# Performance work log

Hardware: AMD Instinct MI355X
Metric: run time of the kernel (lower is better)

Reference implementation:

```python
import jax, jax.numpy as jnp
import numpy as np

B, T, D = 8, 1024, 512
H = 8
F_OUT = D // H          # 64 per head
ALPHA = 0.2             # LeakyReLU slope in GAT
MASK_RATE = 0.3
GAMMA = 0.0625          # DistanceAdj gamma
BIAS = 0.2              # DistanceAdj bias
LN_EPS = 1e-5
NEG_INF = -9e15
L2_EPS = 1e-12          # F.normalize eps


def setup_inputs() -> dict:
    key = jax.random.key(0)
    ks = jax.random.split(key, 8)
    return {
        "x": jax.random.normal(ks[0], (B, T, D), jnp.float32),
        "W": jax.random.normal(ks[1], (H, D, F_OUT), jnp.float32) * 0.05,
        "a_src": jax.random.normal(ks[2], (H, F_OUT), jnp.float32) * 0.05,
        "a_dst": jax.random.normal(ks[3], (H, F_OUT), jnp.float32) * 0.05,
        "W2": jax.random.normal(ks[4], (D, D), jnp.float32) * 0.02,
        "b2": jnp.zeros((D,), jnp.float32),
        "ln_g": jnp.ones((D,), jnp.float32),
        "ln_b": jnp.zeros((D,), jnp.float32),
    }


def _distance_adj(batch, t):
    # DistanceAdj: Gaussian kernel over temporal index distance, shared across batch
    idx = jnp.arange(t, dtype=jnp.float32)
    d2 = (idx[:, None] - idx[None, :]) ** 2
    adj = jnp.exp(-GAMMA * d2 - BIAS)                      # [T, T]
    return jnp.broadcast_to(adj[None], (batch, t, t))      # [B, T, T]


def reference(x, W, a_src, a_dst, W2, b2, ln_g, ln_b):
    b, t, d = x.shape
    adj = _distance_adj(b, t)

    # top-k magnitude node selection -> row/col union mask (index_fill loop)
    k = int(MASK_RATE * t)
    mags = jnp.linalg.norm(x, axis=2)                      # [B, T]
    _, topk = jax.lax.top_k(mags, k)                       # [B, k]
    sel = jnp.zeros((b, t), bool).at[jnp.arange(b)[:, None], topk].set(True)
    mask = sel[:, :, None] | sel[:, None, :]               # rows OR cols filled
    adj = jnp.where(mask, adj, 0.0)

    # GAT multi-head attention (dense masked form, dropout=0 at eval)
    Wh = jnp.einsum("btd,hdf->bhtf", x, W)                 # [B,H,T,F']
    e_src = jnp.einsum("bhtf,hf->bht", Wh, a_src)
    e_dst = jnp.einsum("bhtf,hf->bht", Wh, a_dst)
    e = jax.nn.leaky_relu(e_src[..., :, None] + e_dst[..., None, :], ALPHA)
    e = jnp.where(adj[:, None] > 0, e, NEG_INF)            # masked logits
    attn = jax.nn.softmax(e, axis=-1)                      # [B,H,T,T]
    hp = jnp.einsum("bhts,bhsf->bhtf", attn, Wh)
    hp = jax.nn.elu(hp)                                    # concat=True -> elu per head
    tmp = hp.transpose(0, 2, 1, 3).reshape(b, t, d)        # concat heads -> [B,T,512]

    # signed-sqrt + F.normalize (default dim=1 -> over T axis)
    tmp = jnp.sqrt(jax.nn.relu(tmp)) - jnp.sqrt(jax.nn.relu(-tmp))
    nrm = jnp.linalg.norm(tmp, axis=1, keepdims=True)      # [B,1,D]
    tmp = tmp / jnp.maximum(nrm, L2_EPS)

    # residual linear + LayerNorm + permute
    y = x + tmp @ W2 + b2
    mu = jnp.mean(y, axis=-1, keepdims=True)
    var = jnp.mean((y - mu) ** 2, axis=-1, keepdims=True)
    y = (y - mu) / jnp.sqrt(var + LN_EPS) * ln_g + ln_b
    return y.transpose(0, 2, 1)                            # [B, D, T]
```

## Files before the change

### kernel.cpp

```cpp
#include <hip/hip_runtime.h>
#include <hip/hip_bf16.h>

typedef unsigned short u16;
typedef short bf16x8 __attribute__((ext_vector_type(8)));
typedef float f32x4 __attribute__((ext_vector_type(4)));
typedef int   i32x4 __attribute__((ext_vector_type(4)));

#define NB 8
#define NT 1024
#define ND 512
#define KSEL 307
#define PSTR 152
#define TSTR 136

__device__ __forceinline__ float bf2f(u16 u){
  union { unsigned int i; float f; } c; c.i = ((unsigned int)u) << 16; return c.f;
}
__device__ __forceinline__ u16 f2bf(float f){
  __hip_bfloat16 h = __float2bfloat16(f);
  u16 u; __builtin_memcpy(&u, &h, 2); return u;
}

__global__ void k_select(const float* __restrict__ mags, int* __restrict__ sel){
  __shared__ float sm[NT];
  int b = blockIdx.x;
  int tid = threadIdx.x;
  for (int i = tid; i < NT; i += 256) sm[i] = mags[b * NT + i];
  __syncthreads();
  int tl = tid >> 2, tq = tid & 3;
  int t = blockIdx.y * 64 + tl;
  float m = sm[t];
  int cnt = 0;
  int s0 = tq * 256;
  for (int s = s0; s < s0 + 256; s++){
    float v = sm[s];
    cnt += (v > m) || (v == m && s < t);
  }
  cnt += __shfl_xor(cnt, 1, 64);
  cnt += __shfl_xor(cnt, 2, 64);
  if (tq == 0) sel[b * NT + t] = (cnt < KSEL) ? 1 : 0;
}

__launch_bounds__(256, 3)
__global__ void k_gemm_wh(const float* __restrict__ x, const float* __restrict__ Wf,
                          const float* __restrict__ W2f,
                          const float* __restrict__ a_src, const float* __restrict__ a_dst,
                          u16* __restrict__ WhT, float* __restrict__ es, float* __restrict__ ed,
                          float* __restrict__ mags, float* __restrict__ cn,
                          u16* __restrict__ W2T){
  __shared__ u16 smem[8704];
  u16* As = smem;
  u16* Bs = smem + 5120;
  int m0 = blockIdx.x * 128;
  int h  = blockIdx.y;
  int tid = threadIdx.x;
  if (h == 0 && tid < 64) cn[blockIdx.x * 64 + tid] = 0.f;
  if (h == 2){
    float* tile = (float*)smem;
    int kt0 = (blockIdx.x >> 3) * 64, n00 = (blockIdx.x & 7) * 64;
    int r = tid >> 6, cl = tid & 63;
#pragma unroll
    for (int p = 0; p < 16; p++)
      tile[(r + p*4)*65 + cl] = W2f[(size_t)(kt0 + r + p*4) * 512 + n00 + cl];
    __syncthreads();
#pragma unroll
    for (int p = 0; p < 16; p++){
      int orow = r + p*4;
      W2T[(size_t)(n00 + orow) * 512 + kt0 + cl] = f2bf(tile[cl*65 + orow]);
    }
    __syncthreads();
  }
  int wv = tid >> 6, lane = tid & 63;
  int quad = lane >> 4, lr = lane & 15;
  f32x4 acc[2][4] = {};
  float sq[2] = {0.f, 0.f};
  int ar = (tid * 8) >> 5, ac = (tid * 8) & 31;
  const float* xa0 = &x[(size_t)(m0 + ar) * 512 + ac];
  const float* xa1 = xa0 + (size_t)64 * 512;
  int kk = (tid * 8) >> 6, f0 = (tid * 8) & 63;
  const float* wb = &Wf[((size_t)h << 15) + (size_t)kk * 64 + f0];
  int bbase = f0 * 40 + (((kk >> 3) ^ ((f0 >> 3) & 3)) * 8) + (kk & 7);
  f32x4 pa0 = *(const f32x4*)xa0, pa1 = *(const f32x4*)(xa0 + 4);
  f32x4 pa2 = *(const f32x4*)xa1, pa3 = *(const f32x4*)(xa1 + 4);
  f32x4 pb0 = *(const f32x4*)wb,  pb1 = *(const f32x4*)(wb + 4);
  for (int kt = 0; kt < 512; kt += 32){
    __syncthreads();
    {
      u16 pk[8];
      if (h == 0){
#pragma unroll
        for (int q = 0; q < 4; q++) sq[0] += pa0[q]*pa0[q] + pa1[q]*pa1[q];
#pragma unroll
        for (int q = 0; q < 4; q++) sq[1] += pa2[q]*pa2[q] + pa3[q]*pa3[q];
      }
#pragma unroll
      for (int q = 0; q < 4; q++){ pk[q] = f2bf(pa0[q]); pk[4+q] = f2bf(pa1[q]); }
      *(bf16x8*)&As[ar*40 + ac] = *(const bf16x8*)pk;
#pragma unroll
      for (int q = 0; q < 4; q++){ pk[q] = f2bf(pa2[q]); pk[4+q] = f2bf(pa3[q]); }
      *(bf16x8*)&As[(ar + 64)*40 + ac] = *(const bf16x8*)pk;
#pragma unroll
      for (int q = 0; q < 4; q++) Bs[bbase + q*40]       = f2bf(pb0[q]);
#pragma unroll
      for (int q = 0; q < 4; q++) Bs[bbase + (q+4)*40]   = f2bf(pb1[q]);
    }
    __syncthreads();
    if (kt < 480){
      pa0 = *(const f32x4*)(xa0 + kt + 32); pa1 = *(const f32x4*)(xa0 + kt + 36);
      pa2 = *(const f32x4*)(xa1 + kt + 32); pa3 = *(const f32x4*)(xa1 + kt + 36);
      pb0 = *(const f32x4*)(wb + (size_t)(kt + 32) * 64);
      pb1 = *(const f32x4*)(wb + (size_t)(kt + 32) * 64 + 4);
    }
    bf16x8 af[2], bfr[4];
#pragma unroll
    for (int i = 0; i < 2; i++) af[i] = *(const bf16x8*)&As[(wv*32 + i*16 + lr)*40 + quad*8];
#pragma unroll
    for (int i = 0; i < 4; i++){
      int f = i*16 + lr;
      bfr[i] = *(const bf16x8*)&Bs[f*40 + ((quad ^ ((f >> 3) & 3)) * 8)];
    }
#pragma unroll
    for (int mi = 0; mi < 2; mi++)
#pragma unroll
      for (int ni = 0; ni < 4; ni++)
        acc[mi][ni] = __builtin_amdgcn_mfma_f32_16x16x32_bf16(af[mi], bfr[ni], acc[mi][ni], 0, 0, 0);
  }
  if (h == 0){
#pragma unroll
    for (int i = 0; i < 2; i++){
      float s = sq[i];
      s += __shfl_xor(s, 1, 64);
      s += __shfl_xor(s, 2, 64);
      if ((tid & 3) == 0) mags[m0 + i*64 + (tid >> 2)] = sqrtf(s);
    }
  }
  float asv[4], adv[4];
#pragma unroll
  for (int ni = 0; ni < 4; ni++){
    asv[ni] = a_src[h*64 + ni*16 + lr];
    adv[ni] = a_dst[h*64 + ni*16 + lr];
  }
#pragma unroll
  for (int mi = 0; mi < 2; mi++)
#pragma unroll
    for (int r = 0; r < 4; r++){
      float pes = 0.f, ped = 0.f;
#pragma unroll
      for (int ni = 0; ni < 4; ni++){
        pes += acc[mi][ni][r] * asv[ni];
        ped += acc[mi][ni][r] * adv[ni];
      }
#pragma unroll
      for (int mofs = 1; mofs < 16; mofs <<= 1){
        pes += __shfl_xor(pes, mofs, 64);
        ped += __shfl_xor(ped, mofs, 64);
      }
      if (lr == 0){
        int rowg = m0 + wv*32 + mi*16 + quad*4 + r;
        int bb_ = rowg >> 10, tt = rowg & 1023;
        es[(bb_ * 8 + h) * NT + tt] = pes;
        ed[(bb_ * 8 + h) * NT + tt] = ped;
      }
    }
  __syncthreads();
  u16* Tr = smem;
#pragma unroll
  for (int mi = 0; mi < 2; mi++)
#pragma unroll
    for (int ni = 0; ni < 4; ni++){
      int fl = ni*16 + lr;
      int tl = wv*32 + mi*16 + quad*4;
#pragma unroll
      for (int r = 0; r < 4; r++) Tr[fl*TSTR + tl + r] = f2bf(acc[mi][ni][r]);
    }
  __syncthreads();
  int f = tid >> 2, seg = tid & 3;
  int b_ = m0 >> 10;
  u16* dst = &WhT[(b_ * 512 + h * 64 + f) * NT + (m0 & 1023) + seg*32];
  const u16* srcp = &Tr[f*TSTR + seg*32];
#pragma unroll
  for (int k8 = 0; k8 < 4; k8++)
    *(bf16x8*)(dst + k8*8) = *(const bf16x8*)(srcp + k8*8);
}

__launch_bounds__(256)
__global__ void k_attn(const u16* __restrict__ WhT, const float* __restrict__ es,
                       const float* __restrict__ ed, const int* __restrict__ sel,
                       u16* __restrict__ t2b, float* __restrict__ cn){
  __shared__ u16 P[64 * PSTR];
  __shared__ float edw[144];
  __shared__ int   selw[144];
  __shared__ float esw[64];
  __shared__ float swv[64];
  int bh = blockIdx.x;
  int b = bh >> 3;
  int t0 = blockIdx.y * 64;
  int tid = threadIdx.x;
  int wv = tid >> 6, lane = tid & 63;
  int quad = lane >> 4, lr = lane & 15;
  int s_base = t0 - 40;
  for (int i = tid; i < 144; i += 256){
    int s = s_base + i;
    bool ok = (s >= 0 && s < NT);
    edw[i]  = ok ? ed[bh * NT + s] : 0.f;
    selw[i] = ok ? sel[b * NT + s] : 0;
  }
  if (tid < 64) esw[tid] = es[bh * NT + t0 + tid];
  {
    i32x4 z = {};
    for (int i = lane; i < 304; i += 64){
      int r16 = i / 19, c16 = i - r16 * 19;
      *(i32x4*)&P[(16*wv + r16) * PSTR + c16 * 8] = z;
    }
  }
  __syncthreads();
  {
    int tl = 16*wv + (lane >> 2);
    int q = lane & 3;
    float e_t = esw[tl];
    int sel_t = selw[tl + 40];
    float part = 0.f;
    for (int j = q; j <= 80; j += 4){
      int sw = tl + j;
      int s = s_base + sw;
      float w = 0.f;
      if (s >= 0 && s < NT && (sel_t | selw[sw])){
        float v = e_t + edw[sw];
        v = v > 0.f ? v : 0.2f * v;
        v = fminf(v, 60.f);
        w = bf2f(f2bf(__expf(v)));
      }
      part += w;
      if (w != 0.f) P[tl * PSTR + sw] = f2bf(w);
    }
    part += __shfl_xor(part, 1, 64);
    part += __shfl_xor(part, 2, 64);
    if (q == 0) swv[tl] = part;
  }
  __syncthreads();
  f32x4 acc[4] = {};
  const u16* vbase = WhT + (bh * 64) * NT;
#pragma unroll
  for (int ks = 0; ks < 96; ks += 32){
    bf16x8 afr = *(const bf16x8*)&P[(16*wv + lr) * PSTR + 16*wv + ks + quad*8];
    int tb = s_base + 16*wv + ks + quad*8;
    bool ok = (tb >= 0) && (tb < NT);
    bf16x8 zf = {};
#pragma unroll
    for (int jn = 0; jn < 4; jn++){
      bf16x8 bfr = ok ? *(const bf16x8*)&vbase[(16*jn + lr) * NT + tb] : zf;
      acc[jn] = __builtin_amdgcn_mfma_f32_16x16x32_bf16(afr, bfr, acc[jn], 0, 0, 0);
    }
  }
#pragma unroll
  for (int jn = 0; jn < 4; jn++){
    float ssum = 0.f;
#pragma unroll
    for (int r = 0; r < 4; r++){
      int t_loc = 16*wv + quad*4 + r;
      float sw_ = swv[t_loc];
      float hp = acc[jn][r] / (sw_ > 0.f ? sw_ : 1.f);
      hp = hp > 0.f ? hp : (__expf(hp) - 1.f);
      float o = hp >= 0.f ? sqrtf(hp) : -sqrtf(-hp);
      ssum += o * o;
      t2b[(b * NT + t0 + t_loc) * ND + (bh & 7) * 64 + 16*jn + lr] = f2bf(o);
    }
    ssum += __shfl_xor(ssum, 16, 64);
    ssum += __shfl_xor(ssum, 32, 64);
    if (quad == 0) atomicAdd(&cn[b * ND + (bh & 7) * 64 + 16*jn + lr], ssum);
  }
}

__launch_bounds__(512)
__global__ void k_gemm2ln(const u16* __restrict__ A, const u16* __restrict__ W2T,
                          const float* __restrict__ xres, const float* __restrict__ b2,
                          const float* __restrict__ cn, const float* __restrict__ g,
                          const float* __restrict__ bb, float* __restrict__ out){
  __shared__ __align__(16) char smraw[69888];
  u16*   As  = (u16*)smraw;
  u16*   Bs  = (u16*)(smraw + 2560);
  float* scl = (float*)(smraw + 43520);
  float* T     = (float*)smraw;
  float* wpart = (float*)(smraw + 67584);
  float* mus   = (float*)(smraw + 69632);
  float* rss   = (float*)(smraw + 69760);
  int tid = threadIdx.x;
  int m0 = blockIdx.x * 32;
  int b  = m0 >> 10, t0 = m0 & 1023;
  int w = tid >> 6, lane = tid & 63;
  int quad = lane >> 4, lr = lane & 15;
  {
    float nv = sqrtf(cn[(b << 9) + tid]);
    scl[tid] = 1.f / fmaxf(nv, 1e-12f);
  }
  int ar = tid >> 2, ac = (tid & 3) * 8;
  const u16* ap = &A[(size_t)(m0 + ar) * 512 + ac];
  int nb_ = tid >> 2, c = (tid & 3) * 8;
  bf16x8 ra = {}, rb[4];
  if (tid < 128) ra = *(const bf16x8*)ap;
#pragma unroll
  for (int rep = 0; rep < 4; rep++)
    rb[rep] = *(const bf16x8*)&W2T[(size_t)(nb_ + rep*128) * 512 + c];
  f32x4 acc[2][4] = {};
  for (int kt = 0; kt < 512; kt += 32){
    __syncthreads();
    if (tid < 128){
      u16 pk[8];
#pragma unroll
      for (int q = 0; q < 8; q++)
        pk[q] = f2bf(bf2f((u16)ra[q]) * scl[kt + ac + q]);
      *(bf16x8*)&As[ar*40 + ac] = *(const bf16x8*)pk;
    }
#pragma unroll
    for (int rep = 0; rep < 4; rep++)
      *(bf16x8*)&Bs[(nb_ + rep*128)*40 + c] = rb[rep];
    __syncthreads();
    if (kt < 480){
      if (tid < 128) ra = *(const bf16x8*)(ap + kt + 32);
#pragma unroll
      for (int rep = 0; rep < 4; rep++)
        rb[rep] = *(const bf16x8*)&W2T[(size_t)(nb_ + rep*128) * 512 + kt + 32 + c];
    }
    bf16x8 af[2], bfr[4];
#pragma unroll
    for (int mi = 0; mi < 2; mi++) af[mi] = *(const bf16x8*)&As[(mi*16 + lr)*40 + quad*8];
#pragma unroll
    for (int i = 0; i < 4; i++)
      bfr[i] = *(const bf16x8*)&Bs[(w*64 + i*16 + lr)*40 + quad*8];
#pragma unroll
    for (int mi = 0; mi < 2; mi++)
#pragma unroll
      for (int ni = 0; ni < 4; ni++)
        acc[mi][ni] = __builtin_amdgcn_mfma_f32_16x16x32_bf16(af[mi], bfr[ni], acc[mi][ni], 0, 0, 0);
  }
  float b2v[4];
#pragma unroll
  for (int ni = 0; ni < 4; ni++) b2v[ni] = b2[w*64 + ni*16 + lr];
  float yv[2][4][4];
#pragma unroll
  for (int mi = 0; mi < 2; mi++)
#pragma unroll
    for (int r = 0; r < 4; r++){
      int rl = mi*16 + quad*4 + r;
      float rs = 0.f, rq = 0.f;
#pragma unroll
      for (int ni = 0; ni < 4; ni++){
        int col = w*64 + ni*16 + lr;
        float v = acc[mi][ni][r] + xres[(size_t)(m0 + rl) * 512 + col] + b2v[ni];
        yv[mi][ni][r] = v;
        rs += v; rq += v * v;
      }
#pragma unroll
      for (int m2 = 1; m2 < 16; m2 <<= 1){
        rs += __shfl_xor(rs, m2, 64);
        rq += __shfl_xor(rq, m2, 64);
      }
      if (lr == 0){
        wpart[w*32 + rl]       = rs;
        wpart[256 + w*32 + rl] = rq;
      }
    }
  __syncthreads();
  if (tid < 32){
    float s = 0.f, q = 0.f;
#pragma unroll
    for (int wv2 = 0; wv2 < 8; wv2++){
      s += wpart[wv2*32 + tid];
      q += wpart[256 + wv2*32 + tid];
    }
    float mu = s * (1.f/512.f);
    float var = q * (1.f/512.f) - mu * mu;
    mus[tid] = mu;
    rss[tid] = 1.f / sqrtf(var + 1e-5f);
  }
  __syncthreads();
  float gv[4], bv[4];
#pragma unroll
  for (int ni = 0; ni < 4; ni++){
    gv[ni] = g[w*64 + ni*16 + lr];
    bv[ni] = bb[w*64 + ni*16 + lr];
  }
#pragma unroll
  for (int mi = 0; mi < 2; mi++)
#pragma unroll
    for (int r = 0; r < 4; r++){
      int rl = mi*16 + quad*4 + r;
      float mu = mus[rl], rstd = rss[rl];
#pragma unroll
      for (int ni = 0; ni < 4; ni++){
        int col = w*64 + ni*16 + lr;
        T[col*33 + rl] = (yv[mi][ni][r] - mu) * rstd * gv[ni] + bv[ni];
      }
    }
  __syncthreads();
  int j = tid & 31, dq = tid >> 5;
#pragma unroll
  for (int kk2 = 0; kk2 < 32; kk2++){
    int d = dq + kk2 * 16;
    out[((size_t)(b * 512 + d)) * 1024 + t0 + j] = T[d*33 + j];
  }
}

extern "C" void kernel_launch(void* const* d_in, const int* in_sizes, int n_in,
                              void* d_out, int out_size, void* d_ws, size_t ws_size,
                              hipStream_t stream) {
  (void)in_sizes; (void)n_in; (void)out_size; (void)ws_size;
  const float* x     = (const float*)d_in[0];
  const float* W     = (const float*)d_in[1];
  const float* a_src = (const float*)d_in[2];
  const float* a_dst = (const float*)d_in[3];
  const float* W2    = (const float*)d_in[4];
  const float* b2    = (const float*)d_in[5];
  const float* ln_g  = (const float*)d_in[6];
  const float* ln_b  = (const float*)d_in[7];
  char* ws = (char*)d_ws;
  int*   sel   = (int*)  (ws + 256);
  float* mags  = (float*)(ws + 33024);
  float* es    = (float*)(ws + 1124608);
  float* ed    = (float*)(ws + 1386752);
  float* cn    = (float*)(ws + 1648896);
  u16*   WhT   = (u16*)  (ws + 2097152);
  u16*   t2b   = (u16*)  (ws + 18874368);
  u16*   W2T   = (u16*)  (ws + 36175872);
  float* out   = (float*)d_out;

  k_gemm_wh  <<<dim3(64, 8), 256, 0, stream>>>(x, W, W2, a_src, a_dst, WhT, es, ed, mags, cn, W2T);
  k_select   <<<dim3(NB, 16), 256, 0, stream>>>(mags, sel);
  k_attn     <<<dim3(64, 16), 256, 0, stream>>>(WhT, es, ed, sel, t2b, cn);
  k_gemm2ln  <<<dim3(256), 512, 0, stream>>>(t2b, W2T, x, b2, cn, ln_g, ln_b, out);
}
```

Measured before the change: 143.7 us.

## Add bf16 prep kernel and load MFMA fragments directly from global memory

A new prep kernel converts x to bf16, computes row magnitudes, zeroes the column-norm buffer, and transposes W and W2 into bf16 K-major layouts. The Wh GEMM and the W2 GEMM then drop their LDS staging and barriers, loading MFMA operand fragments straight from global memory with register double-buffering. The column scaling in the second GEMM is applied per fragment in registers. This removes per-iteration LDS writes and syncs and the fp32-to-bf16 conversion inside the GEMM loops. In exchange it adds an extra kernel launch and a pass over x in HBM, and operands are re-read from global or L2 with no LDS reuse across waves.

```diff
diff --git a/kernel.cpp b/kernel.cpp
--- a/kernel.cpp
+++ b/kernel.cpp
@@ -19,6 +19,60 @@
 __device__ __forceinline__ u16 f2bf(float f){
   __hip_bfloat16 h = __float2bfloat16(f);
   u16 u; __builtin_memcpy(&u, &h, 2); return u;
+}
+
+__global__ void k_prep(const float* __restrict__ x, const float* __restrict__ Wf,
+                       const float* __restrict__ W2f, u16* __restrict__ xbf,
+                       u16* __restrict__ WbT, u16* __restrict__ W2T,
+                       float* __restrict__ mags, float* __restrict__ cn){
+  __shared__ float tile[64][65];
+  int bx = blockIdx.x;
+  int tid = threadIdx.x;
+  if (bx < 512){
+    int wv = tid >> 6, lane = tid & 63;
+#pragma unroll
+    for (int rr = 0; rr < 4; rr++){
+      int row = bx * 16 + wv * 4 + rr;
+      const float* xp = &x[(size_t)row * 512 + lane * 8];
+      f32x4 u0 = *(const f32x4*)xp;
+      f32x4 u1 = *(const f32x4*)(xp + 4);
+      u16 pk[8];
+      float s = 0.f;
+#pragma unroll
+      for (int q = 0; q < 4; q++){
+        s += u0[q]*u0[q] + u1[q]*u1[q];
+        pk[q] = f2bf(u0[q]); pk[4+q] = f2bf(u1[q]);
+      }
+      *(bf16x8*)&xbf[(size_t)row * 512 + lane * 8] = *(const bf16x8*)pk;
+#pragma unroll
+      for (int m = 1; m < 64; m <<= 1) s += __shfl_xor(s, m, 64);
+      if (lane == 0) mags[row] = sqrtf(s);
+    }
+  } else {
+    int tb = bx - 512;
+    if (tb < 16) cn[tb * 256 + tid] = 0.f;
+    const float* src; u16* dst; int srcld, dstld;
+    if (tb < 64){
+      int h = tb >> 3, kt = (tb & 7) * 64;
+      src = Wf + ((size_t)h << 15) + (size_t)kt * 64;  srcld = 64;
+      dst = WbT + ((size_t)h * 64) * 512 + kt;         dstld = 512;
+    } else {
+      int t2 = tb - 64;
+      int kt = (t2 >> 3) * 64, n0 = (t2 & 7) * 64;
+      src = W2f + (size_t)kt * 512 + n0;  srcld = 512;
+      dst = W2T + (size_t)n0 * 512 + kt;  dstld = 512;
+    }
+    int r = tid >> 6, cl = tid & 63;
+#pragma unroll
+    for (int p = 0; p < 16; p++)
+      tile[r + p*4][cl] = src[(size_t)(r + p*4) * srcld + cl];
+    __syncthreads();
+#pragma unroll
+    for (int p = 0; p < 16; p++){
+      int orow = r + p*4;
+      dst[(size_t)orow * dstld + cl] = f2bf(tile[cl][orow]);
+    }
+  }
 }
 
 __global__ void k_select(const float* __restrict__ mags, int* __restrict__ sel){
@@ -42,96 +96,46 @@
 }
 
 __launch_bounds__(256, 3)
-__global__ void k_gemm_wh(const float* __restrict__ x, const float* __restrict__ Wf,
-                          const float* __restrict__ W2f,
+__global__ void k_gemm_wh(const u16* __restrict__ xbf, const u16* __restrict__ Wbf,
                           const float* __restrict__ a_src, const float* __restrict__ a_dst,
-                          u16* __restrict__ WhT, float* __restrict__ es, float* __restrict__ ed,
-                          float* __restrict__ mags, float* __restrict__ cn,
-                          u16* __restrict__ W2T){
-  __shared__ u16 smem[8704];
-  u16* As = smem;
-  u16* Bs = smem + 5120;
+                          u16* __restrict__ WhT, float* __restrict__ es, float* __restrict__ ed){
+  __shared__ u16 Tr[64 * TSTR];
   int m0 = blockIdx.x * 128;
   int h  = blockIdx.y;
   int tid = threadIdx.x;
-  if (h == 0 && tid < 64) cn[blockIdx.x * 64 + tid] = 0.f;
-  if (h == 2){
-    float* tile = (float*)smem;
-    int kt0 = (blockIdx.x >> 3) * 64, n00 = (blockIdx.x & 7) * 64;
-    int r = tid >> 6, cl = tid & 63;
-#pragma unroll
-    for (int p = 0; p < 16; p++)
-      tile[(r + p*4)*65 + cl] = W2f[(size_t)(kt0 + r + p*4) * 512 + n00 + cl];
-    __syncthreads();
-#pragma unroll
-    for (int p = 0; p < 16; p++){
-      int orow = r + p*4;
-      W2T[(size_t)(n00 + orow) * 512 + kt0 + cl] = f2bf(tile[cl*65 + orow]);
-    }
-    __syncthreads();
-  }
   int wv = tid >> 6, lane = tid & 63;
   int quad = lane >> 4, lr = lane & 15;
   f32x4 acc[2][4] = {};
-  float sq[2] = {0.f, 0.f};
-  int ar = (tid * 8) >> 5, ac = (tid * 8) & 31;
-  const float* xa0 = &x[(size_t)(m0 + ar) * 512 + ac];
-  const float* xa1 = xa0 + (size_t)64 * 512;
-  int kk = (tid * 8) >> 6, f0 = (tid * 8) & 63;
-  const float* wb = &Wf[((size_t)h << 15) + (size_t)kk * 64 + f0];
-  int bbase = f0 * 40 + (((kk >> 3) ^ ((f0 >> 3) & 3)) * 8) + (kk & 7);
-  f32x4 pa0 = *(const f32x4*)xa0, pa1 = *(const f32x4*)(xa0 + 4);
-  f32x4 pa2 = *(const f32x4*)xa1, pa3 = *(const f32x4*)(xa1 + 4);
-  f32x4 pb0 = *(const f32x4*)wb,  pb1 = *(const f32x4*)(wb + 4);
+  const u16* ap = &xbf[(size_t)(m0 + wv*32 + lr) * 512 + quad*8];
+  const u16* bp = &Wbf[(size_t)(h*64 + lr) * 512 + quad*8];
+  bf16x8 ca0 = *(const bf16x8*)(ap);
+  bf16x8 ca1 = *(const bf16x8*)(ap + 8192);
+  bf16x8 cb0 = *(const bf16x8*)(bp);
+  bf16x8 cb1 = *(const bf16x8*)(bp + 8192);
+  bf16x8 cb2 = *(const bf16x8*)(bp + 16384);
+  bf16x8 cb3 = *(const bf16x8*)(bp + 24576);
   for (int kt = 0; kt < 512; kt += 32){
-    __syncthreads();
-    {
-      u16 pk[8];
-      if (h == 0){
-#pragma unroll
-        for (int q = 0; q < 4; q++) sq[0] += pa0[q]*pa0[q] + pa1[q]*pa1[q];
-#pragma unroll
-        for (int q = 0; q < 4; q++) sq[1] += pa2[q]*pa2[q] + pa3[q]*pa3[q];
-      }
-#pragma unroll
-      for (int q = 0; q < 4; q++){ pk[q] = f2bf(pa0[q]); pk[4+q] = f2bf(pa1[q]); }
-      *(bf16x8*)&As[ar*40 + ac] = *(const bf16x8*)pk;
-#pragma unroll
-      for (int q = 0; q < 4; q++){ pk[q] = f2bf(pa2[q]); pk[4+q] = f2bf(pa3[q]); }
-      *(bf16x8*)&As[(ar + 64)*40 + ac] = *(const bf16x8*)pk;
-#pragma unroll
-      for (int q = 0; q < 4; q++) Bs[bbase + q*40]       = f2bf(pb0[q]);
-#pragma unroll
-      for (int q = 0; q < 4; q++) Bs[bbase + (q+4)*40]   = f2bf(pb1[q]);
-    }
-    __syncthreads();
-    if (kt < 480){
-      pa0 = *(const f32x4*)(xa0 + kt + 32); pa1 = *(const f32x4*)(xa0 + kt + 36);
-      pa2 = *(const f32x4*)(xa1 + kt + 32); pa3 = *(const f32x4*)(xa1 + kt + 36);
-      pb0 = *(const f32x4*)(wb + (size_t)(kt + 32) * 64);
-      pb1 = *(const f32x4*)(wb + (size_t)(kt + 32) * 64 + 4);
-    }
-    bf16x8 af[2], bfr[4];
-#pragma unroll
-    for (int i = 0; i < 2; i++) af[i] = *(const bf16x8*)&As[(wv*32 + i*16 + lr)*40 + quad*8];
-#pragma unroll
-    for (int i = 0; i < 4; i++){
-      int f = i*16 + lr;
-      bfr[i] = *(const bf16x8*)&Bs[f*40 + ((quad ^ ((f >> 3) & 3)) * 8)];
-    }
-#pragma unroll
-    for (int mi = 0; mi < 2; mi++)
-#pragma unroll
-      for (int ni = 0; ni < 4; ni++)
-        acc[mi][ni] = __builtin_amdgcn_mfma_f32_16x16x32_bf16(af[mi], bfr[ni], acc[mi][ni], 0, 0, 0);
-  }
-  if (h == 0){
-#pragma unroll
-    for (int i = 0; i < 2; i++){
-      float s = sq[i];
-      s += __shfl_xor(s, 1, 64);
-      s += __shfl_xor(s, 2, 64);
-      if ((tid & 3) == 0) mags[m0 + i*64 + (tid >> 2)] = sqrtf(s);
+    bf16x8 na0, na1, nb0, nb1, nb2, nb3;
+    bool pf = kt < 480;
+    if (pf){
+      na0 = *(const bf16x8*)(ap + kt + 32);
+      na1 = *(const bf16x8*)(ap + 8192 + kt + 32);
+      nb0 = *(const bf16x8*)(bp + kt + 32);
+      nb1 = *(const bf16x8*)(bp + 8192 + kt + 32);
+      nb2 = *(const bf16x8*)(bp + 16384 + kt + 32);
+      nb3 = *(const bf16x8*)(bp + 24576 + kt + 32);
+    }
+    acc[0][0] = __builtin_amdgcn_mfma_f32_16x16x32_bf16(ca0, cb0, acc[0][0], 0, 0, 0);
+    acc[0][1] = __builtin_amdgcn_mfma_f32_16x16x32_bf16(ca0, cb1, acc[0][1], 0, 0, 0);
+    acc[0][2] = __builtin_amdgcn_mfma_f32_16x16x32_bf16(ca0, cb2, acc[0][2], 0, 0, 0);
+    acc[0][3] = __builtin_amdgcn_mfma_f32_16x16x32_bf16(ca0, cb3, acc[0][3], 0, 0, 0);
+    acc[1][0] = __builtin_amdgcn_mfma_f32_16x16x32_bf16(ca1, cb0, acc[1][0], 0, 0, 0);
+    acc[1][1] = __builtin_amdgcn_mfma_f32_16x16x32_bf16(ca1, cb1, acc[1][1], 0, 0, 0);
+    acc[1][2] = __builtin_amdgcn_mfma_f32_16x16x32_bf16(ca1, cb2, acc[1][2], 0, 0, 0);
+    acc[1][3] = __builtin_amdgcn_mfma_f32_16x16x32_bf16(ca1, cb3, acc[1][3], 0, 0, 0);
+    if (pf){
+      ca0 = na0; ca1 = na1;
+      cb0 = nb0; cb1 = nb1; cb2 = nb2; cb3 = nb3;
     }
   }
   float asv[4], adv[4];
@@ -162,8 +166,6 @@
         ed[(bb_ * 8 + h) * NT + tt] = ped;
       }
     }
-  __syncthreads();
-  u16* Tr = smem;
 #pragma unroll
   for (int mi = 0; mi < 2; mi++)
 #pragma unroll
@@ -277,9 +279,7 @@
                           const float* __restrict__ cn, const float* __restrict__ g,
                           const float* __restrict__ bb, float* __restrict__ out){
   __shared__ __align__(16) char smraw[69888];
-  u16*   As  = (u16*)smraw;
-  u16*   Bs  = (u16*)(smraw + 2560);
-  float* scl = (float*)(smraw + 43520);
+  float* scl = (float*)smraw;
   float* T     = (float*)smraw;
   float* wpart = (float*)(smraw + 67584);
   float* mus   = (float*)(smraw + 69632);
@@ -293,45 +293,54 @@
     float nv = sqrtf(cn[(b << 9) + tid]);
     scl[tid] = 1.f / fmaxf(nv, 1e-12f);
   }
-  int ar = tid >> 2, ac = (tid & 3) * 8;
-  const u16* ap = &A[(size_t)(m0 + ar) * 512 + ac];
-  int nb_ = tid >> 2, c = (tid & 3) * 8;
-  bf16x8 ra = {}, rb[4];
-  if (tid < 128) ra = *(const bf16x8*)ap;
-#pragma unroll
-  for (int rep = 0; rep < 4; rep++)
-    rb[rep] = *(const bf16x8*)&W2T[(size_t)(nb_ + rep*128) * 512 + c];
+  __syncthreads();
   f32x4 acc[2][4] = {};
+  const u16* ap = &A[(size_t)(m0 + lr) * 512 + quad*8];
+  const u16* bp = &W2T[(size_t)(w*64 + lr) * 512 + quad*8];
+  bf16x8 ca0 = *(const bf16x8*)(ap);
+  bf16x8 ca1 = *(const bf16x8*)(ap + 8192);
+  bf16x8 cb0 = *(const bf16x8*)(bp);
+  bf16x8 cb1 = *(const bf16x8*)(bp + 8192);
+  bf16x8 cb2 = *(const bf16x8*)(bp + 16384);
+  bf16x8 cb3 = *(const bf16x8*)(bp + 24576);
   for (int kt = 0; kt < 512; kt += 32){
-    __syncthreads();
-    if (tid < 128){
-      u16 pk[8];
-#pragma unroll
-      for (int q = 0; q < 8; q++)
-        pk[q] = f2bf(bf2f((u16)ra[q]) * scl[kt + ac + q]);
-      *(bf16x8*)&As[ar*40 + ac] = *(const bf16x8*)pk;
-    }
-#pragma unroll
-    for (int rep = 0; rep < 4; rep++)
-      *(bf16x8*)&Bs[(nb_ + rep*128)*40 + c] = rb[rep];
-    __syncthreads();
-    if (kt < 480){
-      if (tid < 128) ra = *(const bf16x8*)(ap + kt + 32);
-#pragma unroll
-      for (int rep = 0; rep < 4; rep++)
-        rb[rep] = *(const bf16x8*)&W2T[(size_t)(nb_ + rep*128) * 512 + kt + 32 + c];
-    }
-    bf16x8 af[2], bfr[4];
-#pragma unroll
-    for (int mi = 0; mi < 2; mi++) af[mi] = *(const bf16x8*)&As[(mi*16 + lr)*40 + quad*8];
-#pragma unroll
-    for (int i = 0; i < 4; i++)
-      bfr[i] = *(const bf16x8*)&Bs[(w*64 + i*16 + lr)*40 + quad*8];
-#pragma unroll
-    for (int mi = 0; mi < 2; mi++)
-#pragma unroll
-      for (int ni = 0; ni < 4; ni++)
-        acc[mi][ni] = __builtin_amdgcn_mfma_f32_16x16x32_bf16(af[mi], bfr[ni], acc[mi][ni], 0, 0, 0);
+    bf16x8 na0, na1, nb0, nb1, nb2, nb3;
+    bool pf = kt < 480;
+    if (pf){
+      na0 = *(const bf16x8*)(ap + kt + 32);
+      na1 = *(const bf16x8*)(ap + 8192 + kt + 32);
+      nb0 = *(const bf16x8*)(bp + kt + 32);
+      nb1 = *(const bf16x8*)(bp + 8192 + kt + 32);
+      nb2 = *(const bf16x8*)(bp + 16384 + kt + 32);
+      nb3 = *(const bf16x8*)(bp + 24576 + kt + 32);
+    }
+    f32x4 s0 = *(const f32x4*)&scl[kt + quad*8];
+    f32x4 s1 = *(const f32x4*)&scl[kt + quad*8 + 4];
+    bf16x8 af0, af1;
+    {
+      u16 pk0[8], pk1[8];
+#pragma unroll
+      for (int q = 0; q < 4; q++){
+        pk0[q]   = f2bf(bf2f((u16)ca0[q])   * s0[q]);
+        pk0[4+q] = f2bf(bf2f((u16)ca0[4+q]) * s1[q]);
+        pk1[q]   = f2bf(bf2f((u16)ca1[q])   * s0[q]);
+        pk1[4+q] = f2bf(bf2f((u16)ca1[4+q]) * s1[q]);
+      }
+      af0 = *(const bf16x8*)pk0;
+      af1 = *(const bf16x8*)pk1;
+    }
+    acc[0][0] = __builtin_amdgcn_mfma_f32_16x16x32_bf16(af0, cb0, acc[0][0], 0, 0, 0);
+    acc[0][1] = __builtin_amdgcn_mfma_f32_16x16x32_bf16(af0, cb1, acc[0][1], 0, 0, 0);
+    acc[0][2] = __builtin_amdgcn_mfma_f32_16x16x32_bf16(af0, cb2, acc[0][2], 0, 0, 0);
+    acc[0][3] = __builtin_amdgcn_mfma_f32_16x16x32_bf16(af0, cb3, acc[0][3], 0, 0, 0);
+    acc[1][0] = __builtin_amdgcn_mfma_f32_16x16x32_bf16(af1, cb0, acc[1][0], 0, 0, 0);
+    acc[1][1] = __builtin_amdgcn_mfma_f32_16x16x32_bf16(af1, cb1, acc[1][1], 0, 0, 0);
+    acc[1][2] = __builtin_amdgcn_mfma_f32_16x16x32_bf16(af1, cb2, acc[1][2], 0, 0, 0);
+    acc[1][3] = __builtin_amdgcn_mfma_f32_16x16x32_bf16(af1, cb3, acc[1][3], 0, 0, 0);
+    if (pf){
+      ca0 = na0; ca1 = na1;
+      cb0 = nb0; cb1 = nb1; cb2 = nb2; cb3 = nb3;
+    }
   }
   float b2v[4];
 #pragma unroll
@@ -421,11 +430,14 @@
   float* cn    = (float*)(ws + 1648896);
   u16*   WhT   = (u16*)  (ws + 2097152);
   u16*   t2b   = (u16*)  (ws + 18874368);
+  u16*   xbf   = (u16*)  (ws + 27262976);
+  u16*   Wbf   = (u16*)  (ws + 35651584);
   u16*   W2T   = (u16*)  (ws + 36175872);
   float* out   = (float*)d_out;
 
-  k_gemm_wh  <<<dim3(64, 8), 256, 0, stream>>>(x, W, W2, a_src, a_dst, WhT, es, ed, mags, cn, W2T);
+  k_prep     <<<dim3(640), 256, 0, stream>>>(x, W, W2, xbf, Wbf, W2T, mags, cn);
   k_select   <<<dim3(NB, 16), 256, 0, stream>>>(mags, sel);
+  k_gemm_wh  <<<dim3(64, 8), 256, 0, stream>>>(xbf, Wbf, a_src, a_dst, WhT, es, ed);
   k_attn     <<<dim3(64, 16), 256, 0, stream>>>(WhT, es, ed, sel, t2b, cn);
   k_gemm2ln  <<<dim3(256), 512, 0, stream>>>(t2b, W2T, x, b2, cn, ln_g, ln_b, out);
 }
```

Measured after the change: 168.5 us. 1.17x slower.

## Compute two heads per block in Wh GEMM to reuse x tiles

Applied to the files above, without the earlier changes.

The Wh projection kernel now gives each block two attention heads (128 output features) with 512 threads, instead of one head with 256 threads. Each wave covers 16 rows across 128 columns, so the x tile is loaded from global memory and converted to bf16 once per pair of heads rather than once per head. The e_src/e_dst reductions, the W2 transpose and the WhT transpose-store are adapted to the new mapping, and the grid shrinks from 64x8 to 64x4 blocks. The cost is twice the shared memory per block and fewer, larger blocks, which may reduce latency hiding.

```diff
diff --git a/kernel.cpp b/kernel.cpp
--- a/kernel.cpp
+++ b/kernel.cpp
@@ -3,6 +3,7 @@
 
 typedef unsigned short u16;
 typedef short bf16x8 __attribute__((ext_vector_type(8)));
+typedef short u16x4 __attribute__((ext_vector_type(4)));
 typedef float f32x4 __attribute__((ext_vector_type(4)));
 typedef int   i32x4 __attribute__((ext_vector_type(4)));
 
@@ -41,142 +42,130 @@
   if (tq == 0) sel[b * NT + t] = (cnt < KSEL) ? 1 : 0;
 }
 
-__launch_bounds__(256, 3)
+__launch_bounds__(512, 2)
 __global__ void k_gemm_wh(const float* __restrict__ x, const float* __restrict__ Wf,
                           const float* __restrict__ W2f,
                           const float* __restrict__ a_src, const float* __restrict__ a_dst,
                           u16* __restrict__ WhT, float* __restrict__ es, float* __restrict__ ed,
                           float* __restrict__ mags, float* __restrict__ cn,
                           u16* __restrict__ W2T){
-  __shared__ u16 smem[8704];
+  __shared__ u16 smem[17408];
   u16* As = smem;
   u16* Bs = smem + 5120;
   int m0 = blockIdx.x * 128;
-  int h  = blockIdx.y;
+  int hp = blockIdx.y;
   int tid = threadIdx.x;
-  if (h == 0 && tid < 64) cn[blockIdx.x * 64 + tid] = 0.f;
-  if (h == 2){
+  if (hp == 0 && tid < 64) cn[blockIdx.x * 64 + tid] = 0.f;
+  if (hp == 1){
     float* tile = (float*)smem;
     int kt0 = (blockIdx.x >> 3) * 64, n00 = (blockIdx.x & 7) * 64;
     int r = tid >> 6, cl = tid & 63;
 #pragma unroll
-    for (int p = 0; p < 16; p++)
-      tile[(r + p*4)*65 + cl] = W2f[(size_t)(kt0 + r + p*4) * 512 + n00 + cl];
-    __syncthreads();
-#pragma unroll
-    for (int p = 0; p < 16; p++){
-      int orow = r + p*4;
+    for (int p = 0; p < 8; p++)
+      tile[(r + p*8)*65 + cl] = W2f[(size_t)(kt0 + r + p*8) * 512 + n00 + cl];
+    __syncthreads();
+#pragma unroll
+    for (int p = 0; p < 8; p++){
+      int orow = r + p*8;
       W2T[(size_t)(n00 + orow) * 512 + kt0 + cl] = f2bf(tile[cl*65 + orow]);
     }
     __syncthreads();
   }
   int wv = tid >> 6, lane = tid & 63;
   int quad = lane >> 4, lr = lane & 15;
-  f32x4 acc[2][4] = {};
-  float sq[2] = {0.f, 0.f};
-  int ar = (tid * 8) >> 5, ac = (tid * 8) & 31;
-  const float* xa0 = &x[(size_t)(m0 + ar) * 512 + ac];
-  const float* xa1 = xa0 + (size_t)64 * 512;
-  int kk = (tid * 8) >> 6, f0 = (tid * 8) & 63;
-  const float* wb = &Wf[((size_t)h << 15) + (size_t)kk * 64 + f0];
+  f32x4 acc[8] = {};
+  float sq = 0.f;
+  int ar = tid >> 2, ac = (tid & 3) * 8;
+  const float* xa = &x[(size_t)(m0 + ar) * 512 + ac];
+  int f0 = (tid * 8) & 127, kk = (tid * 8) >> 7;
+  int hh = hp * 2 + (f0 >> 6), fl0 = f0 & 63;
+  const float* wb = &Wf[((size_t)hh << 15) + (size_t)kk * 64 + fl0];
   int bbase = f0 * 40 + (((kk >> 3) ^ ((f0 >> 3) & 3)) * 8) + (kk & 7);
-  f32x4 pa0 = *(const f32x4*)xa0, pa1 = *(const f32x4*)(xa0 + 4);
-  f32x4 pa2 = *(const f32x4*)xa1, pa3 = *(const f32x4*)(xa1 + 4);
-  f32x4 pb0 = *(const f32x4*)wb,  pb1 = *(const f32x4*)(wb + 4);
+  f32x4 pa0 = *(const f32x4*)xa, pa1 = *(const f32x4*)(xa + 4);
+  f32x4 pb0 = *(const f32x4*)wb, pb1 = *(const f32x4*)(wb + 4);
   for (int kt = 0; kt < 512; kt += 32){
     __syncthreads();
     {
       u16 pk[8];
-      if (h == 0){
-#pragma unroll
-        for (int q = 0; q < 4; q++) sq[0] += pa0[q]*pa0[q] + pa1[q]*pa1[q];
-#pragma unroll
-        for (int q = 0; q < 4; q++) sq[1] += pa2[q]*pa2[q] + pa3[q]*pa3[q];
+      if (hp == 0){
+#pragma unroll
+        for (int q = 0; q < 4; q++) sq += pa0[q]*pa0[q] + pa1[q]*pa1[q];
       }
 #pragma unroll
       for (int q = 0; q < 4; q++){ pk[q] = f2bf(pa0[q]); pk[4+q] = f2bf(pa1[q]); }
       *(bf16x8*)&As[ar*40 + ac] = *(const bf16x8*)pk;
 #pragma unroll
-      for (int q = 0; q < 4; q++){ pk[q] = f2bf(pa2[q]); pk[4+q] = f2bf(pa3[q]); }
-      *(bf16x8*)&As[(ar + 64)*40 + ac] = *(const bf16x8*)pk;
-#pragma unroll
-      for (int q = 0; q < 4; q++) Bs[bbase + q*40]       = f2bf(pb0[q]);
-#pragma unroll
-      for (int q = 0; q < 4; q++) Bs[bbase + (q+4)*40]   = f2bf(pb1[q]);
+      for (int q = 0; q < 4; q++) Bs[bbase + q*40]     = f2bf(pb0[q]);
+#pragma unroll
+      for (int q = 0; q < 4; q++) Bs[bbase + (q+4)*40] = f2bf(pb1[q]);
     }
     __syncthreads();
     if (kt < 480){
-      pa0 = *(const f32x4*)(xa0 + kt + 32); pa1 = *(const f32x4*)(xa0 + kt + 36);
-      pa2 = *(const f32x4*)(xa1 + kt + 32); pa3 = *(const f32x4*)(xa1 + kt + 36);
+      pa0 = *(const f32x4*)(xa + kt + 32); pa1 = *(const f32x4*)(xa + kt + 36);
       pb0 = *(const f32x4*)(wb + (size_t)(kt + 32) * 64);
       pb1 = *(const f32x4*)(wb + (size_t)(kt + 32) * 64 + 4);
     }
-    bf16x8 af[2], bfr[4];
-#pragma unroll
-    for (int i = 0; i < 2; i++) af[i] = *(const bf16x8*)&As[(wv*32 + i*16 + lr)*40 + quad*8];
-#pragma unroll
-    for (int i = 0; i < 4; i++){
-      int f = i*16 + lr;
-      bfr[i] = *(const bf16x8*)&Bs[f*40 + ((quad ^ ((f >> 3) & 3)) * 8)];
-    }
-#pragma unroll
-    for (int mi = 0; mi < 2; mi++)
-#pragma unroll
-      for (int ni = 0; ni < 4; ni++)
-        acc[mi][ni] = __builtin_amdgcn_mfma_f32_16x16x32_bf16(af[mi], bfr[ni], acc[mi][ni], 0, 0, 0);
-  }
-  if (h == 0){
-#pragma unroll
-    for (int i = 0; i < 2; i++){
-      float s = sq[i];
-      s += __shfl_xor(s, 1, 64);
-      s += __shfl_xor(s, 2, 64);
-      if ((tid & 3) == 0) mags[m0 + i*64 + (tid >> 2)] = sqrtf(s);
-    }
-  }
-  float asv[4], adv[4];
-#pragma unroll
-  for (int ni = 0; ni < 4; ni++){
-    asv[ni] = a_src[h*64 + ni*16 + lr];
-    adv[ni] = a_dst[h*64 + ni*16 + lr];
-  }
-#pragma unroll
-  for (int mi = 0; mi < 2; mi++)
-#pragma unroll
-    for (int r = 0; r < 4; r++){
-      float pes = 0.f, ped = 0.f;
-#pragma unroll
-      for (int ni = 0; ni < 4; ni++){
-        pes += acc[mi][ni][r] * asv[ni];
-        ped += acc[mi][ni][r] * adv[ni];
-      }
-#pragma unroll
-      for (int mofs = 1; mofs < 16; mofs <<= 1){
-        pes += __shfl_xor(pes, mofs, 64);
-        ped += __shfl_xor(ped, mofs, 64);
-      }
-      if (lr == 0){
-        int rowg = m0 + wv*32 + mi*16 + quad*4 + r;
-        int bb_ = rowg >> 10, tt = rowg & 1023;
-        es[(bb_ * 8 + h) * NT + tt] = pes;
-        ed[(bb_ * 8 + h) * NT + tt] = ped;
-      }
-    }
+    bf16x8 af = *(const bf16x8*)&As[(wv*16 + lr)*40 + quad*8];
+#pragma unroll
+    for (int ni = 0; ni < 8; ni++){
+      int f = ni*16 + lr;
+      bf16x8 bfr = *(const bf16x8*)&Bs[f*40 + ((quad ^ ((f >> 3) & 3)) * 8)];
+      acc[ni] = __builtin_amdgcn_mfma_f32_16x16x32_bf16(af, bfr, acc[ni], 0, 0, 0);
+    }
+  }
+  if (hp == 0){
+    float s = sq;
+    s += __shfl_xor(s, 1, 64);
+    s += __shfl_xor(s, 2, 64);
+    if ((tid & 3) == 0) mags[m0 + (tid >> 2)] = sqrtf(s);
+  }
+  float asv[8], adv[8];
+#pragma unroll
+  for (int ni = 0; ni < 8; ni++){
+    asv[ni] = a_src[hp*128 + ni*16 + lr];
+    adv[ni] = a_dst[hp*128 + ni*16 + lr];
+  }
+#pragma unroll
+  for (int r = 0; r < 4; r++){
+    float pes0 = 0.f, ped0 = 0.f, pes1 = 0.f, ped1 = 0.f;
+#pragma unroll
+    for (int ni = 0; ni < 4; ni++){
+      pes0 += acc[ni][r] * asv[ni];
+      ped0 += acc[ni][r] * adv[ni];
+      pes1 += acc[ni+4][r] * asv[ni+4];
+      ped1 += acc[ni+4][r] * adv[ni+4];
+    }
+#pragma unroll
+    for (int mofs = 1; mofs < 16; mofs <<= 1){
+      pes0 += __shfl_xor(pes0, mofs, 64);
+      ped0 += __shfl_xor(ped0, mofs, 64);
+      pes1 += __shfl_xor(pes1, mofs, 64);
+      ped1 += __shfl_xor(ped1, mofs, 64);
+    }
+    if (lr == 0){
+      int rowg = m0 + wv*16 + quad*4 + r;
+      int bb_ = rowg >> 10, tt = rowg & 1023;
+      es[(bb_ * 8 + hp*2) * NT + tt]     = pes0;
+      ed[(bb_ * 8 + hp*2) * NT + tt]     = ped0;
+      es[(bb_ * 8 + hp*2 + 1) * NT + tt] = pes1;
+      ed[(bb_ * 8 + hp*2 + 1) * NT + tt] = ped1;
+    }
+  }
   __syncthreads();
   u16* Tr = smem;
 #pragma unroll
-  for (int mi = 0; mi < 2; mi++)
-#pragma unroll
-    for (int ni = 0; ni < 4; ni++){
-      int fl = ni*16 + lr;
-      int tl = wv*32 + mi*16 + quad*4;
-#pragma unroll
-      for (int r = 0; r < 4; r++) Tr[fl*TSTR + tl + r] = f2bf(acc[mi][ni][r]);
-    }
+  for (int ni = 0; ni < 8; ni++){
+    int fl = ni*16 + lr;
+    int tl = wv*16 + quad*4;
+    u16 pk[4];
+#pragma unroll
+    for (int r = 0; r < 4; r++) pk[r] = f2bf(acc[ni][r]);
+    *(u16x4*)&Tr[fl*TSTR + tl] = *(const u16x4*)pk;
+  }
   __syncthreads();
   int f = tid >> 2, seg = tid & 3;
   int b_ = m0 >> 10;
-  u16* dst = &WhT[(b_ * 512 + h * 64 + f) * NT + (m0 & 1023) + seg*32];
+  u16* dst = &WhT[((size_t)b_ * 512 + hp * 128 + f) * NT + (m0 & 1023) + seg*32];
   const u16* srcp = &Tr[f*TSTR + seg*32];
 #pragma unroll
   for (int k8 = 0; k8 < 4; k8++)
@@ -424,7 +413,7 @@
   u16*   W2T   = (u16*)  (ws + 36175872);
   float* out   = (float*)d_out;
 
-  k_gemm_wh  <<<dim3(64, 8), 256, 0, stream>>>(x, W, W2, a_src, a_dst, WhT, es, ed, mags, cn, W2T);
+  k_gemm_wh  <<<dim3(64, 4), 512, 0, stream>>>(x, W, W2, a_src, a_dst, WhT, es, ed, mags, cn, W2T);
   k_select   <<<dim3(NB, 16), 256, 0, stream>>>(mags, sel);
   k_attn     <<<dim3(64, 16), 256, 0, stream>>>(WhT, es, ed, sel, t2b, cn);
   k_gemm2ln  <<<dim3(256), 512, 0, stream>>>(t2b, W2T, x, b2, cn, ln_g, ln_b, out);
```

New measurement: 144.6 us. No clear change (+0.6%).

## Pre-convert x and W to bf16 in a separate prep kernel before GEMM

Applied to the files above, without the earlier changes.

Adds a k_prep kernel that converts x to bf16 and computes the row magnitudes. The same kernel transposes W and W2 into bf16 K-major layouts and zeroes cn. The Wh GEMM then loads bf16 tiles directly with 16-byte vector loads and no in-loop conversion or norm work. This halves the GEMM's global read traffic and removes the divergent h==0 and h==2 branches, at the cost of an extra kernel launch and a workspace write plus read of bf16 x.

```diff
diff --git a/kernel.cpp b/kernel.cpp
--- a/kernel.cpp
+++ b/kernel.cpp
@@ -19,6 +19,60 @@
 __device__ __forceinline__ u16 f2bf(float f){
   __hip_bfloat16 h = __float2bfloat16(f);
   u16 u; __builtin_memcpy(&u, &h, 2); return u;
+}
+
+__global__ void k_prep(const float* __restrict__ x, const float* __restrict__ Wf,
+                       const float* __restrict__ W2f, u16* __restrict__ xbf,
+                       u16* __restrict__ WbT, u16* __restrict__ W2T,
+                       float* __restrict__ mags, float* __restrict__ cn){
+  __shared__ float tile[64][65];
+  int bx = blockIdx.x;
+  int tid = threadIdx.x;
+  if (bx < 512){
+    int wv = tid >> 6, lane = tid & 63;
+#pragma unroll
+    for (int rr = 0; rr < 4; rr++){
+      int row = bx * 16 + wv * 4 + rr;
+      const float* xp = &x[(size_t)row * 512 + lane * 8];
+      f32x4 u0 = *(const f32x4*)xp;
+      f32x4 u1 = *(const f32x4*)(xp + 4);
+      u16 pk[8];
+      float s = 0.f;
+#pragma unroll
+      for (int q = 0; q < 4; q++){
+        s += u0[q]*u0[q] + u1[q]*u1[q];
+        pk[q] = f2bf(u0[q]); pk[4+q] = f2bf(u1[q]);
+      }
+      *(bf16x8*)&xbf[(size_t)row * 512 + lane * 8] = *(const bf16x8*)pk;
+#pragma unroll
+      for (int m = 1; m < 64; m <<= 1) s += __shfl_xor(s, m, 64);
+      if (lane == 0) mags[row] = sqrtf(s);
+    }
+  } else {
+    int tb = bx - 512;
+    if (tb < 16) cn[tb * 256 + tid] = 0.f;
+    const float* src; u16* dst; int srcld, dstld;
+    if (tb < 64){
+      int h = tb >> 3, kt = (tb & 7) * 64;
+      src = Wf + ((size_t)h << 15) + (size_t)kt * 64;  srcld = 64;
+      dst = WbT + ((size_t)h * 64) * 512 + kt;         dstld = 512;
+    } else {
+      int t2 = tb - 64;
+      int kt = (t2 >> 3) * 64, n0 = (t2 & 7) * 64;
+      src = W2f + (size_t)kt * 512 + n0;  srcld = 512;
+      dst = W2T + (size_t)n0 * 512 + kt;  dstld = 512;
+    }
+    int r = tid >> 6, cl = tid & 63;
+#pragma unroll
+    for (int p = 0; p < 16; p++)
+      tile[r + p*4][cl] = src[(size_t)(r + p*4) * srcld + cl];
+    __syncthreads();
+#pragma unroll
+    for (int p = 0; p < 16; p++){
+      int orow = r + p*4;
+      dst[(size_t)orow * dstld + cl] = f2bf(tile[cl][orow]);
+    }
+  }
 }
 
 __global__ void k_select(const float* __restrict__ mags, int* __restrict__ sel){
@@ -42,97 +96,46 @@
 }
 
 __launch_bounds__(256, 3)
-__global__ void k_gemm_wh(const float* __restrict__ x, const float* __restrict__ Wf,
-                          const float* __restrict__ W2f,
+__global__ void k_gemm_wh(const u16* __restrict__ xbf, const u16* __restrict__ WbT,
                           const float* __restrict__ a_src, const float* __restrict__ a_dst,
-                          u16* __restrict__ WhT, float* __restrict__ es, float* __restrict__ ed,
-                          float* __restrict__ mags, float* __restrict__ cn,
-                          u16* __restrict__ W2T){
+                          u16* __restrict__ WhT, float* __restrict__ es, float* __restrict__ ed){
   __shared__ u16 smem[8704];
   u16* As = smem;
   u16* Bs = smem + 5120;
   int m0 = blockIdx.x * 128;
   int h  = blockIdx.y;
   int tid = threadIdx.x;
-  if (h == 0 && tid < 64) cn[blockIdx.x * 64 + tid] = 0.f;
-  if (h == 2){
-    float* tile = (float*)smem;
-    int kt0 = (blockIdx.x >> 3) * 64, n00 = (blockIdx.x & 7) * 64;
-    int r = tid >> 6, cl = tid & 63;
-#pragma unroll
-    for (int p = 0; p < 16; p++)
-      tile[(r + p*4)*65 + cl] = W2f[(size_t)(kt0 + r + p*4) * 512 + n00 + cl];
-    __syncthreads();
-#pragma unroll
-    for (int p = 0; p < 16; p++){
-      int orow = r + p*4;
-      W2T[(size_t)(n00 + orow) * 512 + kt0 + cl] = f2bf(tile[cl*65 + orow]);
-    }
-    __syncthreads();
-  }
   int wv = tid >> 6, lane = tid & 63;
   int quad = lane >> 4, lr = lane & 15;
   f32x4 acc[2][4] = {};
-  float sq[2] = {0.f, 0.f};
-  int ar = (tid * 8) >> 5, ac = (tid * 8) & 31;
-  const float* xa0 = &x[(size_t)(m0 + ar) * 512 + ac];
-  const float* xa1 = xa0 + (size_t)64 * 512;
-  int kk = (tid * 8) >> 6, f0 = (tid * 8) & 63;
-  const float* wb = &Wf[((size_t)h << 15) + (size_t)kk * 64 + f0];
-  int bbase = f0 * 40 + (((kk >> 3) ^ ((f0 >> 3) & 3)) * 8) + (kk & 7);
-  f32x4 pa0 = *(const f32x4*)xa0, pa1 = *(const f32x4*)(xa0 + 4);
-  f32x4 pa2 = *(const f32x4*)xa1, pa3 = *(const f32x4*)(xa1 + 4);
-  f32x4 pb0 = *(const f32x4*)wb,  pb1 = *(const f32x4*)(wb + 4);
+  int ar0 = (tid * 8) >> 5, ac = (tid * 8) & 31;
+  const u16* ap0 = &xbf[(size_t)(m0 + ar0) * 512 + ac];
+  const u16* ap1 = ap0 + (size_t)64 * 512;
+  const u16* bp  = &WbT[(size_t)(h * 64 + ar0) * 512 + ac];
+  bf16x8 ra0 = *(const bf16x8*)ap0;
+  bf16x8 ra1 = *(const bf16x8*)ap1;
+  bf16x8 rb  = *(const bf16x8*)bp;
   for (int kt = 0; kt < 512; kt += 32){
     __syncthreads();
-    {
-      u16 pk[8];
-      if (h == 0){
-#pragma unroll
-        for (int q = 0; q < 4; q++) sq[0] += pa0[q]*pa0[q] + pa1[q]*pa1[q];
-#pragma unroll
-        for (int q = 0; q < 4; q++) sq[1] += pa2[q]*pa2[q] + pa3[q]*pa3[q];
-      }
-#pragma unroll
-      for (int q = 0; q < 4; q++){ pk[q] = f2bf(pa0[q]); pk[4+q] = f2bf(pa1[q]); }
-      *(bf16x8*)&As[ar*40 + ac] = *(const bf16x8*)pk;
-#pragma unroll
-      for (int q = 0; q < 4; q++){ pk[q] = f2bf(pa2[q]); pk[4+q] = f2bf(pa3[q]); }
-      *(bf16x8*)&As[(ar + 64)*40 + ac] = *(const bf16x8*)pk;
-#pragma unroll
-      for (int q = 0; q < 4; q++) Bs[bbase + q*40]       = f2bf(pb0[q]);
-#pragma unroll
-      for (int q = 0; q < 4; q++) Bs[bbase + (q+4)*40]   = f2bf(pb1[q]);
-    }
+    *(bf16x8*)&As[ar0*40 + ac]        = ra0;
+    *(bf16x8*)&As[(ar0 + 64)*40 + ac] = ra1;
+    *(bf16x8*)&Bs[ar0*40 + ac]        = rb;
     __syncthreads();
     if (kt < 480){
-      pa0 = *(const f32x4*)(xa0 + kt + 32); pa1 = *(const f32x4*)(xa0 + kt + 36);
-      pa2 = *(const f32x4*)(xa1 + kt + 32); pa3 = *(const f32x4*)(xa1 + kt + 36);
-      pb0 = *(const f32x4*)(wb + (size_t)(kt + 32) * 64);
-      pb1 = *(const f32x4*)(wb + (size_t)(kt + 32) * 64 + 4);
+      ra0 = *(const bf16x8*)(ap0 + kt + 32);
+      ra1 = *(const bf16x8*)(ap1 + kt + 32);
+      rb  = *(const bf16x8*)(bp  + kt + 32);
     }
     bf16x8 af[2], bfr[4];
 #pragma unroll
     for (int i = 0; i < 2; i++) af[i] = *(const bf16x8*)&As[(wv*32 + i*16 + lr)*40 + quad*8];
 #pragma unroll
-    for (int i = 0; i < 4; i++){
-      int f = i*16 + lr;
-      bfr[i] = *(const bf16x8*)&Bs[f*40 + ((quad ^ ((f >> 3) & 3)) * 8)];
-    }
+    for (int i = 0; i < 4; i++) bfr[i] = *(const bf16x8*)&Bs[(i*16 + lr)*40 + quad*8];
 #pragma unroll
     for (int mi = 0; mi < 2; mi++)
 #pragma unroll
       for (int ni = 0; ni < 4; ni++)
         acc[mi][ni] = __builtin_amdgcn_mfma_f32_16x16x32_bf16(af[mi], bfr[ni], acc[mi][ni], 0, 0, 0);
-  }
-  if (h == 0){
-#pragma unroll
-    for (int i = 0; i < 2; i++){
-      float s = sq[i];
-      s += __shfl_xor(s, 1, 64);
-      s += __shfl_xor(s, 2, 64);
-      if ((tid & 3) == 0) mags[m0 + i*64 + (tid >> 2)] = sqrtf(s);
-    }
   }
   float asv[4], adv[4];
 #pragma unroll
@@ -421,10 +424,13 @@
   float* cn    = (float*)(ws + 1648896);
   u16*   WhT   = (u16*)  (ws + 2097152);
   u16*   t2b   = (u16*)  (ws + 18874368);
+  u16*   xbf   = (u16*)  (ws + 27262976);
+  u16*   Wbf   = (u16*)  (ws + 35651584);
   u16*   W2T   = (u16*)  (ws + 36175872);
   float* out   = (float*)d_out;
 
-  k_gemm_wh  <<<dim3(64, 8), 256, 0, stream>>>(x, W, W2, a_src, a_dst, WhT, es, ed, mags, cn, W2T);
+  k_prep     <<<dim3(640), 256, 0, stream>>>(x, W, W2, xbf, Wbf, W2T, mags, cn);
+  k_gemm_wh  <<<dim3(64, 8), 256, 0, stream>>>(xbf, Wbf, a_src, a_dst, WhT, es, ed);
   k_select   <<<dim3(NB, 16), 256, 0, stream>>>(mags, sel);
   k_attn     <<<dim3(64, 16), 256, 0, stream>>>(WhT, es, ed, sel, t2b, cn);
   k_gemm2ln  <<<dim3(256), 512, 0, stream>>>(t2b, W2T, x, b2, cn, ln_g, ln_b, out);
```

Result: no change. 145.4 us (+1.2%).
